# Kernel optimization log

Hardware: AMD Instinct MI355X
Metric: run time of the kernel (lower is better)

Reference implementation:

```python
import jax, jax.numpy as jnp
import numpy as np

D_MODEL = 1024
EXPAND = 2
HEADDIM = 64
D_STATE = 128
D_CONV = 4
D_INNER = EXPAND * D_MODEL          # 2048
NHEADS = D_INNER // HEADDIM         # 32
CONV_DIM = D_INNER + 2 * D_STATE    # x, B, C share the depthwise conv
EPS = 1e-5


def setup_inputs() -> dict:
    key = jax.random.key(0)
    ks = jax.random.split(key, 8)
    d_in_proj = 2 * D_INNER + 2 * D_STATE + NHEADS
    x = jax.random.normal(ks[0], (2, 2048, D_MODEL), jnp.float32)
    W_in = jax.random.normal(ks[1], (D_MODEL, d_in_proj), jnp.float32) * (D_MODEL ** -0.5)
    conv_w = jax.random.normal(ks[2], (CONV_DIM, D_CONV), jnp.float32) * 0.2
    conv_b = jnp.zeros((CONV_DIM,), jnp.float32)
    # dt init: softplus(dt_bias) in [1e-3, 1e-1]  (inverse-softplus init, as in mamba_ssm)
    dt = jnp.exp(jax.random.uniform(ks[3], (NHEADS,), jnp.float32,
                                    minval=np.log(1e-3), maxval=np.log(1e-1)))
    dt_bias = dt + jnp.log(-jnp.expm1(-dt))
    A_log = jnp.log(jax.random.uniform(ks[4], (NHEADS,), jnp.float32, minval=1.0, maxval=16.0))
    D = jnp.ones((NHEADS,), jnp.float32)
    norm_w = jnp.ones((D_INNER,), jnp.float32)
    W_out = jax.random.normal(ks[5], (D_INNER, D_MODEL), jnp.float32) * (D_INNER ** -0.5)
    return dict(x=x, W_in=W_in, conv_w=conv_w, conv_b=conv_b, dt_bias=dt_bias,
                A_log=A_log, D=D, norm_w=norm_w, W_out=W_out)


def _causal_depthwise_conv(u, w, b):
    # u: (B, L, C), w: (C, K) depthwise, causal (pad K-1 on the left)
    B, L, C = u.shape
    up = jnp.pad(u, ((0, 0), (D_CONV - 1, 0), (0, 0)))
    y = b
    for k in range(D_CONV):
        y = y + up[:, k:k + L, :] * w[:, k]
    return y


def _rms(v):
    return v * jax.lax.rsqrt(jnp.mean(v * v, axis=-1, keepdims=True) + EPS)


def reference(x, W_in, conv_w, conv_b, dt_bias, A_log, D, norm_w, W_out):
    b, l, _ = x.shape
    zxbcdt = x @ W_in                                  # (b, l, 2*d_inner + 2*d_state + nheads)
    z = zxbcdt[..., :D_INNER]
    xBC = zxbcdt[..., D_INNER:D_INNER + CONV_DIM]
    dt = jax.nn.softplus(zxbcdt[..., -NHEADS:] + dt_bias)   # (b, l, h)
    xBC = jax.nn.silu(_causal_depthwise_conv(xBC, conv_w, conv_b))
    xs = xBC[..., :D_INNER].reshape(b, l, NHEADS, HEADDIM)  # (b, l, h, p)
    Bm = xBC[..., D_INNER:D_INNER + D_STATE]                 # (b, l, n)
    Cm = xBC[..., D_INNER + D_STATE:]                        # (b, l, n)
    A = -jnp.exp(A_log)                                      # (h,)
    decay = jnp.exp(dt * A)                                  # (b, l, h)

    def step(h, inp):
        dec_t, dt_t, x_t, B_t, C_t = inp   # (b,h) (b,h) (b,h,p) (b,n) (b,n)
        h = h * dec_t[:, :, None, None] + (dt_t[:, :, None] * x_t)[..., None] * B_t[:, None, None, :]
        y_t = jnp.einsum('bhpn,bn->bhp', h, C_t)
        return h, y_t

    h0 = jnp.zeros((b, NHEADS, HEADDIM, D_STATE), x.dtype)
    xs_t = (decay.transpose(1, 0, 2), dt.transpose(1, 0, 2),
            xs.transpose(1, 0, 2, 3), Bm.transpose(1, 0, 2), Cm.transpose(1, 0, 2))
    _, ys = jax.lax.scan(step, h0, xs_t)                     # ys: (l, b, h, p)
    y = ys.transpose(1, 0, 2, 3) + D[None, None, :, None] * xs
    y = y.reshape(b, l, D_INNER)
    # gated RMSNorm (RMSNormGated in mamba_ssm), then out projection
    y = _rms(y * jax.nn.silu(z)) * norm_w
    out = y @ W_out                                          # (b, l, d_model)
    # wrapper: post RMSNorm (weight freshly initialized to ones) + residual
    return _rms(out) + x
```

## Files before the change

### kernel.cpp

```cpp
#include <hip/hip_runtime.h>
#include <hip/hip_bf16.h>

#define DMODEL 1024
#define DI     2048
#define DSTATE 128
#define NH     32
#define HD     64
#define CONVD  2304
#define LSEQ   2048
#define BATCH  2
#define DPROJ  4384
#define NPAD   4480
#define EPSV   1e-5f
#define QCH    128
#define NCH    16

#define AS1 __attribute__((address_space(1)))
#define AS3 __attribute__((address_space(3)))

typedef __attribute__((ext_vector_type(8))) short bf16x8;
typedef __attribute__((ext_vector_type(4))) float f32x4;

union U4 { ushort4 u; __hip_bfloat16 h[4]; };

__device__ __forceinline__ float bf2f(unsigned short u) {
  union { unsigned int i; float f; } c; c.i = ((unsigned)u) << 16; return c.f;
}
__device__ __forceinline__ ushort4 pack4(float x0, float x1, float x2, float x3) {
  U4 p;
  p.h[0] = __float2bfloat16(x0); p.h[1] = __float2bfloat16(x1);
  p.h[2] = __float2bfloat16(x2); p.h[3] = __float2bfloat16(x3);
  return p.u;
}

__device__ __forceinline__ bf16x8 ldsfrag(const __hip_bfloat16* base, int row, int ke) {
  int byte = row * 256 + ke * 2;
  byte ^= (row & 7) << 4;
  return *reinterpret_cast<const bf16x8*>(reinterpret_cast<const char*>(base) + byte);
}
__device__ __forceinline__ void ldswr4(__hip_bfloat16* base, int row, int col, ushort4 v) {
  int byte = row * 256 + col * 2;
  byte ^= (row & 7) << 4;
  *reinterpret_cast<ushort4*>(reinterpret_cast<char*>(base) + byte) = v;
}
__device__ __forceinline__ ushort4 ldsrd4(const __hip_bfloat16* base, int row, int col) {
  int byte = row * 256 + col * 2;
  byte ^= (row & 7) << 4;
  return *reinterpret_cast<const ushort4*>(reinterpret_cast<const char*>(base) + byte);
}
__device__ __forceinline__ void ldswr8(__hip_bfloat16* base, int row, int colElem,
                                       unsigned lo, unsigned hi) {
  int byte = row * 256 + colElem * 2;
  byte ^= (row & 7) << 4;
  uint2 v; v.x = lo; v.y = hi;
  *reinterpret_cast<uint2*>(reinterpret_cast<char*>(base) + byte) = v;
}
__device__ __forceinline__ bf16x8 frag32(const __hip_bfloat16* base, int row, int g) {
  int byte = row * 64 + (((g ^ (row >> 1)) & 3) << 4);
  return *reinterpret_cast<const bf16x8*>(reinterpret_cast<const char*>(base) + byte);
}

__device__ __forceinline__ void quadtr(unsigned a01, unsigned a23, int ql,
                                       unsigned& w01, unsigned& w23) {
  unsigned y01 = __shfl_xor((int)a01, 1), y23 = __shfl_xor((int)a23, 1);
  unsigned c01 = (ql & 1) ? ((y01 >> 16) | (a01 & 0xFFFF0000u))
                          : ((a01 & 0xFFFFu) | (y01 << 16));
  unsigned c23 = (ql & 1) ? ((y23 >> 16) | (a23 & 0xFFFF0000u))
                          : ((a23 & 0xFFFFu) | (y23 << 16));
  unsigned d01 = __shfl_xor((int)c01, 2), d23 = __shfl_xor((int)c23, 2);
  w01 = (ql & 2) ? d23 : c01;
  w23 = (ql & 2) ? c23 : d01;
}


__global__ __launch_bounds__(256)
void prep_kernel(const float* __restrict__ x, __hip_bfloat16* __restrict__ xbf,
                 const float* __restrict__ W_in, __hip_bfloat16* __restrict__ wtin,
                 const float* __restrict__ W_out, __hip_bfloat16* __restrict__ wtout) {
  __shared__ float tile[32][33];
  const int b = blockIdx.x, tid = threadIdx.x;
  if (b < 4096) {
    int i = b * 256 + tid;
    float4 v = reinterpret_cast<const float4*>(x)[i];
    reinterpret_cast<ushort4*>(xbf)[i] = pack4(v.x, v.y, v.z, v.w);
    return;
  }
  const float* in;
  __hip_bfloat16* outp;
  int R, C, Cpad, n0, k0;
  if (b < 4096 + 4480) {
    int t = b - 4096;
    in = W_in; outp = wtin; R = 1024; C = 4384; Cpad = 4480;
    n0 = (t % 140) * 32; k0 = (t / 140) * 32;
  } else {
    int t = b - 8576;
    in = W_out; outp = wtout; R = 2048; C = 1024; Cpad = 1024;
    n0 = (t % 32) * 32; k0 = (t / 32) * 32;
  }
  int tx = tid & 31, ty = tid >> 5;
#pragma unroll
  for (int j = 0; j < 32; j += 8) {
    int k = k0 + ty + j, n = n0 + tx;
    tile[ty + j][tx] = (n < C) ? in[(size_t)k * C + n] : 0.f;
  }
  __syncthreads();
#pragma unroll
  for (int j = 0; j < 32; j += 8) {
    int n = n0 + ty + j, k = k0 + tx;
    if (n < Cpad) outp[(size_t)n * R + k] = __float2bfloat16(tile[tx][ty + j]);
  }
}


template <int MODE>
__global__ __launch_bounds__(512, 2)
void gemm256_bt(const __hip_bfloat16* __restrict__ A,
                const __hip_bfloat16* __restrict__ Bt,
                __hip_bfloat16* __restrict__ Cout,
                float* __restrict__ dtraw, int K) {
  __shared__ __hip_bfloat16 smA[4][256 * 32];
  __shared__ __hip_bfloat16 smB[4][256 * 32];

  if constexpr (MODE == 0) {
    if (blockIdx.x >= 256) {
      const int bb = blockIdx.x - 256;
      const int bm = (bb / 3) * 128;
      const int bn = 4096 + (bb % 3) * 128;
      const int tid = threadIdx.x;
      const int w8 = tid >> 6, lane = tid & 63;
      const bool act = (w8 < 4);
      const int w = w8 & 3;
      const int wr = (w >> 1) * 64, wc = (w & 1) * 64;
      const int fr = lane & 15, g = lane >> 4;
      const int srow = lane >> 2;
      const int scol = ((lane & 3) ^ ((lane >> 3) & 3)) * 8;
      __hip_bfloat16* mA = &smA[0][0];
      __hip_bfloat16* mB = &smB[0][0];

      f32x4 acc[4][4];
#pragma unroll
      for (int m = 0; m < 4; ++m)
#pragma unroll
        for (int n = 0; n < 4; ++n) acc[m][n] = (f32x4){0.f, 0.f, 0.f, 0.f};

      const __hip_bfloat16* aSrc = A + (size_t)(bm + srow) * K + scol;
      const __hip_bfloat16* bSrc = Bt + (size_t)(bn + srow) * K + scol;

      auto STG = [&](int buf, int k0) {
#pragma unroll
        for (int j = 0; j < 2; ++j) {
          int ro = w * 32 + j * 16;
          __builtin_amdgcn_global_load_lds((const AS1 void*)(aSrc + (size_t)ro * K + k0),
                                           (AS3 void*)(&mA[buf * 4096 + ro * 32]), 16, 0, 0);
          __builtin_amdgcn_global_load_lds((const AS1 void*)(bSrc + (size_t)ro * K + k0),
                                           (AS3 void*)(&mB[buf * 4096 + ro * 32]), 16, 0, 0);
        }
      };

      if (act) STG(0, 0);
      __syncthreads();
      const int nt = K >> 5;
      int cur = 0;
      for (int kt = 0; kt < nt; ++kt) {
        if (act) {
          if (kt + 1 < nt) STG(cur ^ 1, (kt + 1) << 5);
          bf16x8 af[4], bfv[4];
#pragma unroll
          for (int m = 0; m < 4; ++m) af[m] = frag32(&mA[cur * 4096], wr + m * 16 + fr, g);
#pragma unroll
          for (int n = 0; n < 4; ++n) bfv[n] = frag32(&mB[cur * 4096], wc + n * 16 + fr, g);
#pragma unroll
          for (int m = 0; m < 4; ++m)
#pragma unroll
            for (int n = 0; n < 4; ++n)
              acc[m][n] = __builtin_amdgcn_mfma_f32_16x16x32_bf16(af[m], bfv[n], acc[m][n], 0, 0, 0);
        }
        __syncthreads();
        cur ^= 1;
      }

      if (act) {
        const int r4 = g * 4;
        const int cn = lane & 15;
#pragma unroll
        for (int m = 0; m < 4; ++m)
#pragma unroll
          for (int n = 0; n < 4; ++n) {
            int row = bm + wr + m * 16 + r4;
            int col = bn + wc + n * 16 + cn;
            __hip_bfloat16* cp = Cout + (size_t)row * NPAD + col;
#pragma unroll
            for (int j = 0; j < 4; ++j) {
              float v = acc[m][n][j];
              cp[(size_t)j * NPAD] = __float2bfloat16(v);
              if (col >= DI + CONVD && col < DPROJ)
                dtraw[(size_t)(row + j) * NH + (col - (DI + CONVD))] = v;
            }
          }
      }
      return;
    }
  }

  int bm, bn, kbase, Kp;
  if constexpr (MODE == 0) {
    const int xcd = blockIdx.x & 7;
    const int i = blockIdx.x >> 3;
    bm = (xcd * 2 + (i & 1)) * 256;
    bn = (i >> 1) * 256;
    kbase = 0; Kp = K;
  } else {
    const int s = blockIdx.x >> 6;
    const int bb = blockIdx.x & 63;
    const int xcd = bb & 7;
    const int i = bb >> 3;
    bm = (xcd * 2 + (i & 1)) * 256;
    bn = (i >> 1) * 256;
    Kp = K >> 2; kbase = s * Kp;
  }
  const int tid = threadIdx.x;
  const int w = tid >> 6, lane = tid & 63;
  const int wm = w >> 2, wn = w & 3;
  const int fr = lane & 15, g = lane >> 4;
  const int srow = tid >> 2;
  const int sc = (((tid & 3) ^ ((srow >> 1) & 3)) << 3);

  f32x4 acc[8][4];
#pragma unroll
  for (int m = 0; m < 8; ++m)
#pragma unroll
    for (int n = 0; n < 4; ++n) acc[m][n] = (f32x4){0.f, 0.f, 0.f, 0.f};

  const __hip_bfloat16* aS = A + (size_t)(bm + srow) * K + kbase + sc;
  const __hip_bfloat16* bS = Bt + (size_t)(bn + srow) * K + kbase + sc;
  const int dbase = w * 512;

  auto STAGE = [&](int buf, int kt) {
    const int k0 = kt << 5;
#pragma unroll
    for (int j = 0; j < 2; ++j) {
      __builtin_amdgcn_global_load_lds((const AS1 void*)(aS + (size_t)(j * 128) * K + k0),
                                       (AS3 void*)(&smA[buf][j * 4096 + dbase]), 16, 0, 0);
      __builtin_amdgcn_global_load_lds((const AS1 void*)(bS + (size_t)(j * 128) * K + k0),
                                       (AS3 void*)(&smB[buf][j * 4096 + dbase]), 16, 0, 0);
    }
  };

  const int nt = Kp >> 5;
  STAGE(0, 0);
  STAGE(1, 1);
  for (int kt = 0; kt < nt; ++kt) {
    const int cur = kt & 3;
    if (kt + 2 < nt) {
      STAGE((kt + 2) & 3, kt + 2);
      asm volatile("s_waitcnt vmcnt(8)" ::: "memory");
    } else if (kt + 1 < nt) {
      asm volatile("s_waitcnt vmcnt(4)" ::: "memory");
    } else {
      asm volatile("s_waitcnt vmcnt(0)" ::: "memory");
    }
    __builtin_amdgcn_s_barrier();
    __builtin_amdgcn_s_setprio(1);
    bf16x8 af[8], bfv[4];
#pragma unroll
    for (int m = 0; m < 8; ++m)
      af[m] = frag32(&smA[cur][0], wm * 128 + m * 16 + fr, g);
#pragma unroll
    for (int n = 0; n < 4; ++n)
      bfv[n] = frag32(&smB[cur][0], wn * 64 + n * 16 + fr, g);
#pragma unroll
    for (int m = 0; m < 8; ++m)
#pragma unroll
      for (int n = 0; n < 4; ++n)
        acc[m][n] = __builtin_amdgcn_mfma_f32_16x16x32_bf16(af[m], bfv[n], acc[m][n], 0, 0, 0);
    __builtin_amdgcn_s_setprio(0);
  }

  const int rb = g * 4;
#pragma unroll
  for (int m = 0; m < 8; ++m)
#pragma unroll
    for (int n = 0; n < 4; ++n) {
      int row = bm + wm * 128 + m * 16 + rb;
      int col = bn + wn * 64 + n * 16 + fr;
      if constexpr (MODE == 0) {
        __hip_bfloat16* cp = Cout + (size_t)row * NPAD + col;
#pragma unroll
        for (int j = 0; j < 4; ++j)
          cp[(size_t)j * NPAD] = __float2bfloat16(acc[m][n][j]);
      } else {
        __hip_bfloat16* cp = Cout + (size_t)(blockIdx.x >> 6) * 4194304 +
                             (size_t)row * DMODEL + col;
#pragma unroll
        for (int j = 0; j < 4; ++j)
          cp[(size_t)j * DMODEL] = __float2bfloat16(acc[m][n][j]);
      }
    }
}


__global__ __launch_bounds__(256)
void conv_stats_kernel(const __hip_bfloat16* __restrict__ zxb,
                       const float* __restrict__ cw,
                       const float* __restrict__ cb,
                       __hip_bfloat16* __restrict__ xbc,
                       const float* __restrict__ dtraw, const float* __restrict__ dt_bias,
                       const float* __restrict__ A_log,
                       float* __restrict__ csb, float* __restrict__ dtc,
                       float* __restrict__ swb, float* __restrict__ cumdecb,
                       float* __restrict__ pbuf) {
  if (blockIdx.x >= 1152) {
    int w = threadIdx.x >> 6, lane = threadIdx.x & 63;
    int bid = (blockIdx.x - 1152) * 4 + w;
    int c = bid & (NCH - 1);
    int h = (bid >> 4) & 31;
    int b = bid >> 9;
    int t0 = c * QCH;
    float a = expf(A_log[h]);
    float bias = dt_bias[h];
    const float* dtp = dtraw + ((size_t)b * LSEQ + t0) * NH + h;
    float r0 = dtp[lane * NH] + bias;
    float r1 = dtp[(64 + lane) * NH] + bias;
    float v0 = (r0 > 20.f) ? r0 : log1pf(expf(r0));
    float v1 = (r1 > 20.f) ? r1 : log1pf(expf(r1));
    float s0 = v0;
#pragma unroll
    for (int off = 1; off < 64; off <<= 1) {
      float tv = __shfl_up(s0, off);
      if (lane >= off) s0 += tv;
    }
    float T0 = __shfl(s0, 63);
    float s1 = v1;
#pragma unroll
    for (int off = 1; off < 64; off <<= 1) {
      float tv = __shfl_up(s1, off);
      if (lane >= off) s1 += tv;
    }
    float cs1 = s1 + T0;
    float Tt = __shfl(s1, 63) + T0;
    size_t base = (size_t)bid * 128;
    csb[base + lane] = s0;        csb[base + 64 + lane] = cs1;
    dtc[base + lane] = v0;        dtc[base + 64 + lane] = v1;
    swb[base + lane] = v0 * expf(-a * (Tt - s0));
    swb[base + 64 + lane] = v1 * expf(-a * (Tt - cs1));
    cumdecb[base + lane] = expf(-a * s0);
    cumdecb[base + 64 + lane] = expf(-a * cs1);
    if (lane == 0) pbuf[bid] = expf(-a * Tt);
    return;
  }
  int idx = blockIdx.x * 256 + threadIdx.x;
  int c4 = idx % (CONVD / 4);
  int bl8 = idx / (CONVD / 4);
  int l0 = (bl8 % (LSEQ / 8)) * 8;
  int b = bl8 / (LSEQ / 8);
  int c0 = c4 * 4;
  const __hip_bfloat16* src = zxb + (size_t)b * LSEQ * NPAD + DI + c0;

  float wv[4][4];
#pragma unroll
  for (int j = 0; j < 4; ++j)
    *reinterpret_cast<float4*>(wv[j]) = *reinterpret_cast<const float4*>(cw + (c0 + j) * 4);
  float bias[4];
  *reinterpret_cast<float4*>(bias) = *reinterpret_cast<const float4*>(cb + c0);

  float hist[11][4];
#pragma unroll
  for (int r = 0; r < 11; ++r) {
    int row = l0 - 3 + r;
    if (row >= 0) {
      ushort4 v = *reinterpret_cast<const ushort4*>(src + (size_t)row * NPAD);
      hist[r][0] = bf2f(v.x); hist[r][1] = bf2f(v.y);
      hist[r][2] = bf2f(v.z); hist[r][3] = bf2f(v.w);
    } else {
#pragma unroll
      for (int j = 0; j < 4; ++j) hist[r][j] = 0.f;
    }
  }

#pragma unroll
  for (int t = 0; t < 8; ++t) {
    float acc[4];
#pragma unroll
    for (int j = 0; j < 4; ++j) {
      float a = bias[j];
      a = fmaf(wv[j][0], hist[t + 0][j], a);
      a = fmaf(wv[j][1], hist[t + 1][j], a);
      a = fmaf(wv[j][2], hist[t + 2][j], a);
      a = fmaf(wv[j][3], hist[t + 3][j], a);
      acc[j] = a / (1.f + expf(-a));
    }
    *reinterpret_cast<ushort4*>(xbc + ((size_t)b * LSEQ + l0 + t) * CONVD + c0) =
        pack4(acc[0], acc[1], acc[2], acc[3]);
  }
}


__global__ __launch_bounds__(256, 2)
void ssd_mfma_local(const __hip_bfloat16* __restrict__ bxc,
                    const float* __restrict__ csb, const float* __restrict__ dtc,
                    const float* __restrict__ swb,
                    const float* __restrict__ A_log, const float* __restrict__ Dparm,
                    __hip_bfloat16* __restrict__ y, __hip_bfloat16* __restrict__ sbuf) {
  __shared__ __hip_bfloat16 T_B[128 * 128];
  __shared__ __hip_bfloat16 T_C[128 * 128];
  __shared__ __hip_bfloat16 T_X[64 * 128];

  const int bid = blockIdx.x;
  const int c = bid & (NCH - 1);
  const int h = (bid >> 4) & 31;
  const int b = bid >> 9;
  const int tid = threadIdx.x;
  const int w = tid >> 6, lane = tid & 63;
  const int q = lane >> 2, ql = lane & 3;
  const int t0 = c * QCH;
  const __hip_bfloat16* xc = bxc + (size_t)b * LSEQ * CONVD;
  const float a = expf(A_log[h]);
  const float Dh = Dparm[h];

  {
    const int rsub = lane >> 4;
    const int ch = lane & 15;
#pragma unroll
    for (int j = 0; j < 8; ++j) {
      int row = w * 32 + j * 4 + rsub;
      int sc_ = ch ^ (row & 7);
      const __hip_bfloat16* pB = xc + (size_t)(t0 + row) * CONVD + DI + sc_ * 8;
      __builtin_amdgcn_global_load_lds((const AS1 void*)pB,
                                       (AS3 void*)(T_B + (w * 32 + j * 4) * 128), 16, 0, 0);
      __builtin_amdgcn_global_load_lds((const AS1 void*)(pB + DSTATE),
                                       (AS3 void*)(T_C + (w * 32 + j * 4) * 128), 16, 0, 0);
    }
  }
#pragma unroll
  for (int r = 0; r < 8; ++r) {
    int gidx = w * 128 + q * 8 + r;
    int tb = (gidx & 31) * 4;
    int pb = (gidx >> 5) * 4;
    int t = tb + ql;
    ushort4 xv = *reinterpret_cast<const ushort4*>(xc + (size_t)(t0 + t) * CONVD + h * HD + pb);
    unsigned a01 = (unsigned)xv.x | ((unsigned)xv.y << 16);
    unsigned a23 = (unsigned)xv.z | ((unsigned)xv.w << 16);
    unsigned w01, w23;
    quadtr(a01, a23, ql, w01, w23);
    ldswr8(T_X, pb + ql, tb, w01, w23);
  }
  __syncthreads();

  const int fr = lane & 15;
  const int fk = (lane >> 4) * 8;
  const int rb = (lane >> 4) * 4;

  const int sR0 = (w >> 1) * 64, tC0 = (w & 1) * 64;
  f32x4 g[4][4];
#pragma unroll
  for (int m = 0; m < 4; ++m)
#pragma unroll
    for (int n = 0; n < 4; ++n) g[m][n] = (f32x4){0.f, 0.f, 0.f, 0.f};
  for (int kk = 0; kk < 128; kk += 32) {
    bf16x8 af[4], bfv[4];
#pragma unroll
    for (int m = 0; m < 4; ++m) af[m] = ldsfrag(T_B, sR0 + m * 16 + fr, kk + fk);
#pragma unroll
    for (int n = 0; n < 4; ++n) bfv[n] = ldsfrag(T_C, tC0 + n * 16 + fr, kk + fk);
#pragma unroll
    for (int m = 0; m < 4; ++m)
#pragma unroll
      for (int n = 0; n < 4; ++n)
        g[m][n] = __builtin_amdgcn_mfma_f32_16x16x32_bf16(af[m], bfv[n], g[m][n], 0, 0, 0);
  }
  __syncthreads();

  {
    const float* swp = swb + (size_t)bid * 128;
#pragma unroll
    for (int r = 0; r < 16; ++r) {
      int gidx = w * 256 + q * 16 + r;
      int tb = (gidx & 31) * 4;
      int nb = (gidx >> 5) * 4;
      int t = tb + ql;
      ushort4 bv = ldsrd4(T_B, t, nb);
      float wt = swp[t];
      ushort4 sv = pack4(bf2f(bv.x) * wt, bf2f(bv.y) * wt, bf2f(bv.z) * wt, bf2f(bv.w) * wt);
      unsigned a01 = (unsigned)sv.x | ((unsigned)sv.y << 16);
      unsigned a23 = (unsigned)sv.z | ((unsigned)sv.w << 16);
      unsigned w01, w23;
      quadtr(a01, a23, ql, w01, w23);
      ldswr8(T_C, nb + ql, tb, w01, w23);
    }
  }
  __syncthreads();

  {
    const float* csp = csb + (size_t)bid * 128;
    const float* dtp = dtc + (size_t)bid * 128;
#pragma unroll
    for (int m = 0; m < 4; ++m) {
      int sb0 = sR0 + m * 16 + rb;
      float cs_s[4], dt_s[4];
#pragma unroll
      for (int j = 0; j < 4; ++j) { cs_s[j] = csp[sb0 + j]; dt_s[j] = dtp[sb0 + j]; }
#pragma unroll
      for (int n = 0; n < 4; ++n) {
        int tt = tC0 + n * 16 + fr;
        float cst = csp[tt];
        float vv[4];
#pragma unroll
        for (int j = 0; j < 4; ++j) {
          int s = sb0 + j;
          float e = __expf(-a * (cst - cs_s[j])) * dt_s[j];
          float pv = (s <= tt) ? g[m][n][j] * e : 0.f;
          vv[j] = pv + ((s == tt) ? Dh : 0.f);
        }
        ldswr4(T_B, tt, sb0, pack4(vv[0], vv[1], vv[2], vv[3]));
      }
    }
  }
  __syncthreads();

  {
    int tR0 = w * 32;
    f32x4 yac[2][4];
#pragma unroll
    for (int m = 0; m < 2; ++m)
#pragma unroll
      for (int n = 0; n < 4; ++n) yac[m][n] = (f32x4){0.f, 0.f, 0.f, 0.f};
    for (int kk = 0; kk < 128; kk += 32) {
      bf16x8 af[2], bfv[4];
#pragma unroll
      for (int m = 0; m < 2; ++m) af[m] = ldsfrag(T_B, tR0 + m * 16 + fr, kk + fk);
#pragma unroll
      for (int n = 0; n < 4; ++n) bfv[n] = ldsfrag(T_X, n * 16 + fr, kk + fk);
#pragma unroll
      for (int m = 0; m < 2; ++m)
#pragma unroll
        for (int n = 0; n < 4; ++n)
          yac[m][n] = __builtin_amdgcn_mfma_f32_16x16x32_bf16(af[m], bfv[n], yac[m][n], 0, 0, 0);
    }
#pragma unroll
    for (int m = 0; m < 2; ++m)
#pragma unroll
      for (int n = 0; n < 4; ++n) {
        int trow = tR0 + m * 16 + rb;
        int pc = n * 16 + fr;
        __hip_bfloat16* yp = y + ((size_t)b * LSEQ + t0 + trow) * DI + h * HD + pc;
#pragma unroll
        for (int j = 0; j < 4; ++j)
          yp[(size_t)j * DI] = __float2bfloat16(yac[m][n][j]);
      }
  }

  {
    int pR0 = (w >> 1) * 32, nC0 = (w & 1) * 64;
    f32x4 sac[2][4];
#pragma unroll
    for (int m = 0; m < 2; ++m)
#pragma unroll
      for (int n = 0; n < 4; ++n) sac[m][n] = (f32x4){0.f, 0.f, 0.f, 0.f};
    for (int kk = 0; kk < 128; kk += 32) {
      bf16x8 af[2], bfv[4];
#pragma unroll
      for (int m = 0; m < 2; ++m) af[m] = ldsfrag(T_X, pR0 + m * 16 + fr, kk + fk);
#pragma unroll
      for (int n = 0; n < 4; ++n) bfv[n] = ldsfrag(T_C, nC0 + n * 16 + fr, kk + fk);
#pragma unroll
      for (int m = 0; m < 2; ++m)
#pragma unroll
        for (int n = 0; n < 4; ++n)
          sac[m][n] = __builtin_amdgcn_mfma_f32_16x16x32_bf16(af[m], bfv[n], sac[m][n], 0, 0, 0);
    }
    __hip_bfloat16* sg = sbuf + (size_t)bid * 8192;
#pragma unroll
    for (int m = 0; m < 2; ++m)
#pragma unroll
      for (int n = 0; n < 4; ++n) {
        int p = pR0 + m * 16 + rb;
        int nn = nC0 + n * 16 + fr;
#pragma unroll
        for (int j = 0; j < 4; ++j)
          sg[(size_t)(p + j) * 128 + nn] = __float2bfloat16(sac[m][n][j]);
      }
  }
}


__global__ void ssd_prop_kernel(__hip_bfloat16* __restrict__ sbuf,
                                const float* __restrict__ pbuf) {
  int idx = blockIdx.x * 256 + threadIdx.x;
  int bh = idx >> 13;
  int e = idx & 8191;
  __hip_bfloat16* base = sbuf + (size_t)bh * NCH * 8192 + e;
  const float* pb = pbuf + bh * NCH;
  float hs = 0.f;
  for (int cc = 0; cc < NCH; ++cc) {
    float sc = __bfloat162float(base[(size_t)cc * 8192]);
    base[(size_t)cc * 8192] = __float2bfloat16(hs);
    hs = fmaf(hs, pb[cc], sc);
  }
}


__global__ __launch_bounds__(256, 4)
void ssd_mfma_corr(const __hip_bfloat16* __restrict__ bxc, const __hip_bfloat16* __restrict__ sbuf,
                   const float* __restrict__ cumdecb, __hip_bfloat16* __restrict__ y) {
  const int bid = (blockIdx.x / 15) * 16 + 1 + (blockIdx.x % 15);
  const int h = (bid >> 4) & 31;
  const int b = bid >> 9;
  const int tid = threadIdx.x;
  const int w = tid >> 6, lane = tid & 63;
  const int t0 = (bid & (NCH - 1)) * QCH;
  const __hip_bfloat16* xc = bxc + (size_t)b * LSEQ * CONVD;
  const __hip_bfloat16* hsb = sbuf + (size_t)bid * 8192;
  const int fr = lane & 15;
  const int fk = (lane >> 4) * 8;
  const int rb = (lane >> 4) * 4;
  const int tR0 = w * 32;

  f32x4 ac[2][4];
#pragma unroll
  for (int m = 0; m < 2; ++m)
#pragma unroll
    for (int n = 0; n < 4; ++n) ac[m][n] = (f32x4){0.f, 0.f, 0.f, 0.f};

#pragma unroll
  for (int kk = 0; kk < 128; kk += 32) {
    bf16x8 af[2], bfv[4];
#pragma unroll
    for (int m = 0; m < 2; ++m)
      af[m] = *reinterpret_cast<const bf16x8*>(
          xc + (size_t)(t0 + tR0 + m * 16 + fr) * CONVD + DI + DSTATE + kk + fk);
#pragma unroll
    for (int n = 0; n < 4; ++n)
      bfv[n] = *reinterpret_cast<const bf16x8*>(hsb + (size_t)(n * 16 + fr) * 128 + kk + fk);
#pragma unroll
    for (int m = 0; m < 2; ++m)
#pragma unroll
      for (int n = 0; n < 4; ++n)
        ac[m][n] = __builtin_amdgcn_mfma_f32_16x16x32_bf16(af[m], bfv[n], ac[m][n], 0, 0, 0);
  }

  const float* cdp = cumdecb + (size_t)bid * 128;
#pragma unroll
  for (int m = 0; m < 2; ++m) {
    int trow = tR0 + m * 16 + rb;
    float cd[4];
#pragma unroll
    for (int j = 0; j < 4; ++j) cd[j] = cdp[trow + j];
#pragma unroll
    for (int n = 0; n < 4; ++n) {
      int pc = n * 16 + fr;
      __hip_bfloat16* yp = y + ((size_t)b * LSEQ + t0 + trow) * DI + h * HD + pc;
#pragma unroll
      for (int j = 0; j < 4; ++j) {
        float old = __bfloat162float(yp[(size_t)j * DI]);
        yp[(size_t)j * DI] = __float2bfloat16(old + cd[j] * ac[m][n][j]);
      }
    }
  }
}


__global__ __launch_bounds__(256)
void gate_rms_kernel(const __hip_bfloat16* __restrict__ y, const __hip_bfloat16* __restrict__ zxb,
                     const float* __restrict__ nw, __hip_bfloat16* __restrict__ g) {
  int row = blockIdx.x;
  int t = threadIdx.x;
  int c0 = t * 8;
  const __hip_bfloat16* yr = y + (size_t)row * DI + c0;
  const __hip_bfloat16* zr = zxb + (size_t)row * NPAD + c0;
  ushort4 y0 = *reinterpret_cast<const ushort4*>(yr);
  ushort4 y1 = *reinterpret_cast<const ushort4*>(yr + 4);
  ushort4 z0 = *reinterpret_cast<const ushort4*>(zr);
  ushort4 z1 = *reinterpret_cast<const ushort4*>(zr + 4);
  float zf[8] = {bf2f(z0.x), bf2f(z0.y), bf2f(z0.z), bf2f(z0.w),
                 bf2f(z1.x), bf2f(z1.y), bf2f(z1.z), bf2f(z1.w)};
  float yf[8] = {bf2f(y0.x), bf2f(y0.y), bf2f(y0.z), bf2f(y0.w),
                 bf2f(y1.x), bf2f(y1.y), bf2f(y1.z), bf2f(y1.w)};
  float v[8];
  float ss = 0.f;
#pragma unroll
  for (int j = 0; j < 8; ++j) {
    float z = zf[j];
    float vv = yf[j] * (z / (1.f + expf(-z)));
    v[j] = vv;
    ss += vv * vv;
  }
#pragma unroll
  for (int off = 32; off; off >>= 1) ss += __shfl_down(ss, off);
  __shared__ float red[4];
  if ((t & 63) == 0) red[t >> 6] = ss;
  __syncthreads();
  float tot = red[0] + red[1] + red[2] + red[3];
  float rstd = rsqrtf(tot * (1.f / DI) + EPSV);
  float4 na = *reinterpret_cast<const float4*>(nw + c0);
  float4 nb = *reinterpret_cast<const float4*>(nw + c0 + 4);
  ushort4 o0 = pack4(v[0] * rstd * na.x, v[1] * rstd * na.y,
                     v[2] * rstd * na.z, v[3] * rstd * na.w);
  ushort4 o1v = pack4(v[4] * rstd * nb.x, v[5] * rstd * nb.y,
                      v[6] * rstd * nb.z, v[7] * rstd * nb.w);
  ushort4* gp = reinterpret_cast<ushort4*>(g + (size_t)row * DI + c0);
  gp[0] = o0;
  gp[1] = o1v;
}


__global__ __launch_bounds__(256)
void final_rms_add(const __hip_bfloat16* __restrict__ o1p, const float* __restrict__ x,
                   float* __restrict__ out) {
  int row = blockIdx.x;
  int t = threadIdx.x;
  int c0 = t * 4;
  size_t off = (size_t)row * DMODEL + c0;
  float4 o = {0.f, 0.f, 0.f, 0.f};
#pragma unroll
  for (int s = 0; s < 4; ++s) {
    ushort4 p = *reinterpret_cast<const ushort4*>(o1p + (size_t)s * 4194304 + off);
    o.x += bf2f(p.x); o.y += bf2f(p.y); o.z += bf2f(p.z); o.w += bf2f(p.w);
  }
  float ss = o.x * o.x + o.y * o.y + o.z * o.z + o.w * o.w;
#pragma unroll
  for (int off2 = 32; off2; off2 >>= 1) ss += __shfl_down(ss, off2);
  __shared__ float red[4];
  if ((t & 63) == 0) red[t >> 6] = ss;
  __syncthreads();
  float tot = red[0] + red[1] + red[2] + red[3];
  float rstd = rsqrtf(tot * (1.f / DMODEL) + EPSV);
  float4 xv = *reinterpret_cast<const float4*>(x + off);
  float4 r;
  r.x = o.x * rstd + xv.x;
  r.y = o.y * rstd + xv.y;
  r.z = o.z * rstd + xv.z;
  r.w = o.w * rstd + xv.w;
  *reinterpret_cast<float4*>(out + off) = r;
}


extern "C" void kernel_launch(void* const* d_in, const int* in_sizes, int n_in,
                              void* d_out, int out_size, void* d_ws, size_t ws_size,
                              hipStream_t stream) {
  const float* x       = (const float*)d_in[0];
  const float* W_in    = (const float*)d_in[1];
  const float* conv_w  = (const float*)d_in[2];
  const float* conv_b  = (const float*)d_in[3];
  const float* dt_bias = (const float*)d_in[4];
  const float* A_log   = (const float*)d_in[5];
  const float* Dp      = (const float*)d_in[6];
  const float* norm_w  = (const float*)d_in[7];
  const float* W_out   = (const float*)d_in[8];
  float* out = (float*)d_out;

  float* zxF  = (float*)d_ws;
  __hip_bfloat16* zxb = (__hip_bfloat16*)zxF;
  __hip_bfloat16* o1p = zxb;
  float* xbcF = zxF + (size_t)18350080;
  __hip_bfloat16* xbc = (__hip_bfloat16*)xbcF;
  float* ybufF = xbcF + (size_t)9437184;
  __hip_bfloat16* ybuf = (__hip_bfloat16*)ybufF;
  float* dtraw = ybufF + (size_t)8388608;
  float* cumdecb = dtraw + (size_t)131072;
  __hip_bfloat16* xbf   = (__hip_bfloat16*)(cumdecb + 131072);
  __hip_bfloat16* wtin  = xbf + (size_t)4194304;
  __hip_bfloat16* wtout = wtin + (size_t)4587520;
  float* pbuf = (float*)(wtout + (size_t)2097152);
  float* csb  = pbuf + 1024;
  float* dtc  = csb + (size_t)131072;
  float* swb  = dtc + (size_t)131072;
  __hip_bfloat16* sbuf = xbf;
  __hip_bfloat16* gbf = xbf;

  prep_kernel<<<10624, 256, 0, stream>>>(x, xbf, W_in, wtin, W_out, wtout);

  gemm256_bt<0><<<352, 512, 0, stream>>>(xbf, wtin, zxb, dtraw, 1024);

  conv_stats_kernel<<<1408, 256, 0, stream>>>(zxb, conv_w, conv_b, xbc,
                                              dtraw, dt_bias, A_log,
                                              csb, dtc, swb, cumdecb, pbuf);

  ssd_mfma_local<<<1024, 256, 0, stream>>>(xbc, csb, dtc, swb, A_log, Dp, ybuf, sbuf);
  ssd_prop_kernel<<<2048, 256, 0, stream>>>(sbuf, pbuf);
  ssd_mfma_corr<<<960, 256, 0, stream>>>(xbc, sbuf, cumdecb, ybuf);

  gate_rms_kernel<<<4096, 256, 0, stream>>>(ybuf, zxb, norm_w, gbf);

  gemm256_bt<1><<<256, 512, 0, stream>>>(gbf, wtout, o1p, nullptr, 2048);

  final_rms_add<<<4096, 256, 0, stream>>>(o1p, x, out);
}
```

Before: 186.6 us.

## Fold tail GEMM tiles into main blocks instead of separate extra blocks

The in-projection GEMM used 96 extra blocks, each running only 4 of 8 waves, for the 128-wide tail columns (dt and padding). Those tail tiles now run as a second phase inside the first 96 main blocks, with all 8 waves active. The grid shrinks from 352 to 256 blocks so it fits one wave of CUs and avoids a partial second wave. The cost is that those 96 blocks run longer than the others, which can make the kernel's finish time uneven.

```diff
diff --git a/kernel.cpp b/kernel.cpp
--- a/kernel.cpp
+++ b/kernel.cpp
@@ -120,87 +120,6 @@
                 float* __restrict__ dtraw, int K) {
   __shared__ __hip_bfloat16 smA[4][256 * 32];
   __shared__ __hip_bfloat16 smB[4][256 * 32];
-
-  if constexpr (MODE == 0) {
-    if (blockIdx.x >= 256) {
-      const int bb = blockIdx.x - 256;
-      const int bm = (bb / 3) * 128;
-      const int bn = 4096 + (bb % 3) * 128;
-      const int tid = threadIdx.x;
-      const int w8 = tid >> 6, lane = tid & 63;
-      const bool act = (w8 < 4);
-      const int w = w8 & 3;
-      const int wr = (w >> 1) * 64, wc = (w & 1) * 64;
-      const int fr = lane & 15, g = lane >> 4;
-      const int srow = lane >> 2;
-      const int scol = ((lane & 3) ^ ((lane >> 3) & 3)) * 8;
-      __hip_bfloat16* mA = &smA[0][0];
-      __hip_bfloat16* mB = &smB[0][0];
-
-      f32x4 acc[4][4];
-#pragma unroll
-      for (int m = 0; m < 4; ++m)
-#pragma unroll
-        for (int n = 0; n < 4; ++n) acc[m][n] = (f32x4){0.f, 0.f, 0.f, 0.f};
-
-      const __hip_bfloat16* aSrc = A + (size_t)(bm + srow) * K + scol;
-      const __hip_bfloat16* bSrc = Bt + (size_t)(bn + srow) * K + scol;
-
-      auto STG = [&](int buf, int k0) {
-#pragma unroll
-        for (int j = 0; j < 2; ++j) {
-          int ro = w * 32 + j * 16;
-          __builtin_amdgcn_global_load_lds((const AS1 void*)(aSrc + (size_t)ro * K + k0),
-                                           (AS3 void*)(&mA[buf * 4096 + ro * 32]), 16, 0, 0);
-          __builtin_amdgcn_global_load_lds((const AS1 void*)(bSrc + (size_t)ro * K + k0),
-                                           (AS3 void*)(&mB[buf * 4096 + ro * 32]), 16, 0, 0);
-        }
-      };
-
-      if (act) STG(0, 0);
-      __syncthreads();
-      const int nt = K >> 5;
-      int cur = 0;
-      for (int kt = 0; kt < nt; ++kt) {
-        if (act) {
-          if (kt + 1 < nt) STG(cur ^ 1, (kt + 1) << 5);
-          bf16x8 af[4], bfv[4];
-#pragma unroll
-          for (int m = 0; m < 4; ++m) af[m] = frag32(&mA[cur * 4096], wr + m * 16 + fr, g);
-#pragma unroll
-          for (int n = 0; n < 4; ++n) bfv[n] = frag32(&mB[cur * 4096], wc + n * 16 + fr, g);
-#pragma unroll
-          for (int m = 0; m < 4; ++m)
-#pragma unroll
-            for (int n = 0; n < 4; ++n)
-              acc[m][n] = __builtin_amdgcn_mfma_f32_16x16x32_bf16(af[m], bfv[n], acc[m][n], 0, 0, 0);
-        }
-        __syncthreads();
-        cur ^= 1;
-      }
-
-      if (act) {
-        const int r4 = g * 4;
-        const int cn = lane & 15;
-#pragma unroll
-        for (int m = 0; m < 4; ++m)
-#pragma unroll
-          for (int n = 0; n < 4; ++n) {
-            int row = bm + wr + m * 16 + r4;
-            int col = bn + wc + n * 16 + cn;
-            __hip_bfloat16* cp = Cout + (size_t)row * NPAD + col;
-#pragma unroll
-            for (int j = 0; j < 4; ++j) {
-              float v = acc[m][n][j];
-              cp[(size_t)j * NPAD] = __float2bfloat16(v);
-              if (col >= DI + CONVD && col < DPROJ)
-                dtraw[(size_t)(row + j) * NH + (col - (DI + CONVD))] = v;
-            }
-          }
-      }
-      return;
-    }
-  }
 
   int bm, bn, kbase, Kp;
   if constexpr (MODE == 0) {
@@ -296,6 +215,71 @@
           cp[(size_t)j * DMODEL] = __float2bfloat16(acc[m][n][j]);
       }
     }
+
+  if constexpr (MODE == 0) {
+    if (blockIdx.x >= 96) return;
+    const int bb = blockIdx.x;
+    const int bm2 = (bb / 3) * 128;
+    const int bn2 = 4096 + (bb % 3) * 128;
+    const int wm2 = w >> 2, wn2 = w & 3;
+    __hip_bfloat16* mA = &smA[0][0];
+    __hip_bfloat16* mB = &smB[0][0];
+
+    f32x4 ac2[4][2];
+#pragma unroll
+    for (int m = 0; m < 4; ++m)
+#pragma unroll
+      for (int n = 0; n < 2; ++n) ac2[m][n] = (f32x4){0.f, 0.f, 0.f, 0.f};
+
+    const __hip_bfloat16* aS2 = A + (size_t)(bm2 + srow) * K + sc;
+    const __hip_bfloat16* bS2 = Bt + (size_t)(bn2 + srow) * K + sc;
+
+    auto STG = [&](int buf, int k0) {
+      __builtin_amdgcn_global_load_lds((const AS1 void*)(aS2 + k0),
+                                       (AS3 void*)(&mA[buf * 4096 + dbase]), 16, 0, 0);
+      __builtin_amdgcn_global_load_lds((const AS1 void*)(bS2 + k0),
+                                       (AS3 void*)(&mB[buf * 4096 + dbase]), 16, 0, 0);
+    };
+
+    STG(0, 0);
+    __syncthreads();
+    const int nt2 = K >> 5;
+    int cur = 0;
+    for (int kt = 0; kt < nt2; ++kt) {
+      if (kt + 1 < nt2) STG(cur ^ 1, (kt + 1) << 5);
+      bf16x8 af[4], bfv[2];
+#pragma unroll
+      for (int m = 0; m < 4; ++m)
+        af[m] = frag32(&mA[cur * 4096], wm2 * 64 + m * 16 + fr, g);
+#pragma unroll
+      for (int n = 0; n < 2; ++n)
+        bfv[n] = frag32(&mB[cur * 4096], wn2 * 32 + n * 16 + fr, g);
+#pragma unroll
+      for (int m = 0; m < 4; ++m)
+#pragma unroll
+        for (int n = 0; n < 2; ++n)
+          ac2[m][n] = __builtin_amdgcn_mfma_f32_16x16x32_bf16(af[m], bfv[n], ac2[m][n], 0, 0, 0);
+      __syncthreads();
+      cur ^= 1;
+    }
+
+    const int cn = lane & 15;
+#pragma unroll
+    for (int m = 0; m < 4; ++m)
+#pragma unroll
+      for (int n = 0; n < 2; ++n) {
+        int row = bm2 + wm2 * 64 + m * 16 + rb;
+        int col = bn2 + wn2 * 32 + n * 16 + cn;
+        __hip_bfloat16* cp = Cout + (size_t)row * NPAD + col;
+#pragma unroll
+        for (int j = 0; j < 4; ++j) {
+          float v = ac2[m][n][j];
+          cp[(size_t)j * NPAD] = __float2bfloat16(v);
+          if (col >= DI + CONVD && col < DPROJ)
+            dtraw[(size_t)(row + j) * NH + (col - (DI + CONVD))] = v;
+        }
+      }
+  }
 }
 
 
@@ -769,7 +753,7 @@
 
   prep_kernel<<<10624, 256, 0, stream>>>(x, xbf, W_in, wtin, W_out, wtout);
 
-  gemm256_bt<0><<<352, 512, 0, stream>>>(xbf, wtin, zxb, dtraw, 1024);
+  gemm256_bt<0><<<256, 512, 0, stream>>>(xbf, wtin, zxb, dtraw, 1024);
 
   conv_stats_kernel<<<1408, 256, 0, stream>>>(zxb, conv_w, conv_b, xbc,
                                               dtraw, dt_bias, A_log,
```

After: 182.6 us. 1.02x faster.
